# Kernel tuning notes

Hardware: AMD Instinct MI355X
Metric: run time of the kernel (lower is better)

Reference implementation:

```python
import jax, jax.numpy as jnp
import numpy as np

N_NODES = 50000
N_EDGES = 800000
N_GRAPHS = 128
HIDDEN = 64
HEADS = 2
OUT = 4
NEG_SLOPE = 0.2
ALPHA_FLAG = 0.05


def _gat_conv(x, src, dst, W, a_src, a_dst, b):
    # PyG GATConv, concat=False (mean over heads), self-loops already appended.
    N = x.shape[0]
    H, C = a_src.shape
    xh = (x @ W).reshape(N, H, C)                       # [N,H,C]
    s_src = (xh * a_src).sum(-1)                        # [N,H]
    s_dst = (xh * a_dst).sum(-1)                        # [N,H]
    e = s_src[src] + s_dst[dst]                         # [E,H]
    e = jnp.where(e > 0, e, NEG_SLOPE * e)              # LeakyReLU(0.2)
    emax = jax.ops.segment_max(e, dst, num_segments=N)  # per-dst softmax max
    emax = jnp.where(jnp.isfinite(emax), emax, 0.0)
    p = jnp.exp(e - emax[dst])
    denom = jax.ops.segment_sum(p, dst, num_segments=N)
    alpha = p / (denom[dst] + 1e-16)                    # [E,H]
    out = jax.ops.segment_sum(alpha[:, :, None] * xh[src], dst, num_segments=N)
    return out.mean(axis=1) + b                         # [N,HIDDEN]


def setup_inputs() -> dict:
    key = jax.random.key(0)
    ks = jax.random.split(key, 32)
    f = lambda k, shape, s=0.1: (jax.random.normal(k, shape) * s).astype(jnp.float32)
    inp = {}
    inp['x_all'] = jax.random.normal(ks[0], (N_NODES, 8), dtype=jnp.float32)
    inp['climber'] = jax.random.normal(ks[1], (N_GRAPHS, 4), dtype=jnp.float32)
    inp['edge_index'] = jax.random.randint(ks[2], (2, N_EDGES), 0, N_NODES)
    inp['batch'] = jnp.sort(jax.random.randint(ks[3], (N_NODES,), 0, N_GRAPHS))
    H = HIDDEN
    inp['W_in'] = f(ks[4], (6, H)); inp['b_in'] = jnp.zeros((H,), jnp.float32)
    inp['W_c'] = f(ks[5], (4, H)); inp['b_c'] = jnp.zeros((H,), jnp.float32)
    inp['W_f1'] = f(ks[6], (H, 2 * H)); inp['b_f1'] = jnp.zeros((2 * H,), jnp.float32)
    inp['W_f2'] = f(ks[7], (H, 2 * H)); inp['b_f2'] = jnp.zeros((2 * H,), jnp.float32)
    inp['W_g1'] = f(ks[8], (H, HEADS * H)); inp['a_src1'] = f(ks[9], (HEADS, H)); inp['a_dst1'] = f(ks[10], (HEADS, H)); inp['b_g1'] = jnp.zeros((H,), jnp.float32)
    inp['W_g2'] = f(ks[11], (H, HEADS * H)); inp['a_src2'] = f(ks[12], (HEADS, H)); inp['a_dst2'] = f(ks[13], (HEADS, H)); inp['b_g2'] = jnp.zeros((H,), jnp.float32)
    inp['W_cl1'] = f(ks[14], (H, H)); inp['b_cl1'] = jnp.zeros((H,), jnp.float32)
    inp['W_cl2'] = f(ks[15], (H, OUT)); inp['b_cl2'] = jnp.zeros((OUT,), jnp.float32)
    inp['W_fh1'] = f(ks[16], (2, 8), 0.001); inp['b_fh1'] = jnp.zeros((8,), jnp.float32)
    inp['W_fh2'] = f(ks[17], (8, OUT), 0.001); inp['b_fh2'] = jnp.zeros((OUT,), jnp.float32)
    return inp


def reference(x_all, climber, edge_index, batch, W_in, b_in, W_c, b_c,
              W_f1, b_f1, W_f2, b_f2,
              W_g1, a_src1, a_dst1, b_g1,
              W_g2, a_src2, a_dst2, b_g2,
              W_cl1, b_cl1, W_cl2, b_cl2,
              W_fh1, b_fh1, W_fh2, b_fh2):
    N = x_all.shape[0]
    flags = x_all[:, -2:]
    x = x_all[:, :-2]
    # climber embedding (eval mode -> dropout is identity)
    c = jax.nn.relu(climber @ W_c + b_c)                 # [G,H]
    x = x @ W_in + b_in                                  # [N,H]
    # FiLM 1
    gb = c @ W_f1 + b_f1
    gamma, beta = jnp.split(gb, 2, axis=-1)
    x = x * (1.0 + gamma[batch]) + beta[batch]
    # add self-loops (PyG GATConv default)
    loop = jnp.arange(N, dtype=edge_index.dtype)
    src = jnp.concatenate([edge_index[0], loop])
    dst = jnp.concatenate([edge_index[1], loop])
    x = jax.nn.relu(_gat_conv(x, src, dst, W_g1, a_src1, a_dst1, b_g1))
    # FiLM 2
    gb = c @ W_f2 + b_f2
    gamma, beta = jnp.split(gb, 2, axis=-1)
    x = x * (1.0 + gamma[batch]) + beta[batch]
    x = jax.nn.relu(_gat_conv(x, src, dst, W_g2, a_src2, a_dst2, b_g2))
    logits_main = jax.nn.relu(x @ W_cl1 + b_cl1) @ W_cl2 + b_cl2
    logits_flag = jax.nn.relu(flags @ W_fh1 + b_fh1) @ W_fh2 + b_fh2
    return logits_main + ALPHA_FLAG * logits_flag
```

## Files before the change

kernel.cpp:

```cpp
#include <hip/hip_runtime.h>
#include <hip/hip_fp16.h>

#define NEG_SLOPE 0.2f
#define ALPHA_FLAG 0.05f

typedef _Float16 h2t __attribute__((ext_vector_type(2)));
union h2u { unsigned u; h2t h; __half2 hh; float f; };
static __device__ __forceinline__ h2t u_as_h2(unsigned u) { h2u c; c.u = u; return c.h; }
static __device__ __forceinline__ float h2_as_f(__half2 h) { h2u c; c.hh = h; return c.f; }
static __device__ __forceinline__ h2t f_as_h2(float f) { h2u c; c.f = f; return c.h; }

static inline size_t align256(size_t x) { return (x + 255) & ~(size_t)255; }

__global__ void prep_kernel(const float* __restrict__ climber,
                            const float* __restrict__ W_c, const float* __restrict__ b_c,
                            const float* __restrict__ W_f1, const float* __restrict__ b_f1,
                            const float* __restrict__ W_f2, const float* __restrict__ b_f2,
                            float* __restrict__ gb1, float* __restrict__ gb2) {
    __shared__ float c_sh[64];
    int g = blockIdx.x, t = threadIdx.x;
    if (t < 64) {
        float acc = b_c[t];
#pragma unroll
        for (int k = 0; k < 4; ++k) acc = fmaf(climber[g * 4 + k], W_c[k * 64 + t], acc);
        c_sh[t] = fmaxf(acc, 0.f);
    }
    __syncthreads();
    float a1 = b_f1[t], a2 = b_f2[t];
#pragma unroll 8
    for (int h = 0; h < 64; ++h) {
        float cv = c_sh[h];
        a1 = fmaf(cv, W_f1[h * 128 + t], a1);
        a2 = fmaf(cv, W_f2[h * 128 + t], a2);
    }
    gb1[g * 128 + t] = a1;
    gb2[g * 128 + t] = a2;
}

__global__ void hist_kernel(const int* __restrict__ dst, int E,
                            int* __restrict__ counts, int* __restrict__ ranks) {
    int i4 = (blockIdx.x * blockDim.x + threadIdx.x) * 4;
    if (i4 + 3 < E) {
        int4 d = *(const int4*)&dst[i4];
        int4 r;
        r.x = atomicAdd(&counts[d.x], 1);
        r.y = atomicAdd(&counts[d.y], 1);
        r.z = atomicAdd(&counts[d.z], 1);
        r.w = atomicAdd(&counts[d.w], 1);
        *(int4*)&ranks[i4] = r;
    } else {
        for (int u = 0; u < 4; ++u)
            if (i4 + u < E) ranks[i4 + u] = atomicAdd(&counts[dst[i4 + u]], 1);
    }
}

#define SCAN_CHUNK 1024
__global__ void scan_kernel(const int* __restrict__ counts, int* __restrict__ row_ptr, int N) {
    __shared__ int sh[256];
    int b = blockIdx.x, t = threadIdx.x;
    int pre = 0;
    for (int i0 = t * 4; i0 < b * SCAN_CHUNK; i0 += 1024) {
        int4 v = *(const int4*)&counts[i0];
        pre += v.x + v.y + v.z + v.w + 4;
    }
    sh[t] = pre;
    __syncthreads();
#pragma unroll
    for (int off = 128; off; off >>= 1) {
        if (t < off) sh[t] += sh[t + off];
        __syncthreads();
    }
    int base = sh[0];
    __syncthreads();
    int idx0 = b * SCAN_CHUNK + t * 4;
    int c[4];
    if (idx0 + 3 < N) {
        int4 v = *(const int4*)&counts[idx0];
        c[0] = v.x + 1; c[1] = v.y + 1; c[2] = v.z + 1; c[3] = v.w + 1;
    } else {
#pragma unroll
        for (int u = 0; u < 4; ++u) c[u] = (idx0 + u < N) ? counts[idx0 + u] + 1 : 0;
    }
    int s = c[0] + c[1] + c[2] + c[3];
    sh[t] = s;
    __syncthreads();
#pragma unroll
    for (int off = 1; off < 256; off <<= 1) {
        int add = (t >= off) ? sh[t - off] : 0;
        __syncthreads();
        sh[t] += add;
        __syncthreads();
    }
    int run = base + sh[t] - s;
#pragma unroll
    for (int u = 0; u < 4; ++u) {
        if (idx0 + u < N) {
            row_ptr[idx0 + u] = run;
            run += c[u];
            if (idx0 + u == N - 1) row_ptr[N] = run;
        }
    }
}

__global__ void scatter_kernel(const int* __restrict__ src, const int* __restrict__ dst,
                               const int* __restrict__ ranks, const int* __restrict__ counts,
                               const int* __restrict__ row_ptr,
                               int Eh, int N, int* __restrict__ csr_src) {
    int t = blockIdx.x * blockDim.x + threadIdx.x;
    if (t < Eh) {
        int2 s2 = *(const int2*)&src[t * 2];
        int2 d2 = *(const int2*)&dst[t * 2];
        int2 r2 = *(const int2*)&ranks[t * 2];
        csr_src[row_ptr[d2.x] + r2.x] = s2.x;
        csr_src[row_ptr[d2.y] + r2.y] = s2.y;
    } else {
        int i = t - Eh;
        if (i < N) csr_src[row_ptr[i] + counts[i]] = i;
    }
}

#define XH_NB 32
__global__ __launch_bounds__(256, 4) void xh_kernel(
    const __half* __restrict__ xhalf, const float* __restrict__ W_g,
    const float* __restrict__ a_src, const float* __restrict__ a_dst,
    __half* __restrict__ xh, float* __restrict__ s_src, float* __restrict__ s_dst,
    int N, int in_mode,
    const float* __restrict__ x_all, const int* __restrict__ batch,
    const float* __restrict__ W_in, const float* __restrict__ b_in,
    const float* __restrict__ gb1) {
    __shared__ float x_sh[XH_NB * 64];
    __shared__ float win_sh[6 * 64 + 64];
    int t = threadIdx.x;
    int base = blockIdx.x * XH_NB;
    if (in_mode) {
        for (int i = t; i < 448; i += 256)
            win_sh[i] = (i < 384) ? W_in[i] : b_in[i - 384];
        __syncthreads();
        int nd = t >> 3;
        int jb = (t & 7) * 8;
        int n = base + nd;
        if (n < N) {
            float4 a = *(const float4*)&x_all[(size_t)n * 8];
            float2 b = *(const float2*)&x_all[(size_t)n * 8 + 4];
            float xa[6] = {a.x, a.y, a.z, a.w, b.x, b.y};
            int g = batch[n];
            const float* gbrow = &gb1[g * 128];
#pragma unroll
            for (int jj = 0; jj < 8; ++jj) {
                int j = jb + jj;
                float acc = win_sh[384 + j];
#pragma unroll
                for (int k = 0; k < 6; ++k) acc = fmaf(xa[k], win_sh[k * 64 + j], acc);
                x_sh[nd * 64 + j] = acc * (1.f + gbrow[j]) + gbrow[64 + j];
            }
        } else {
#pragma unroll
            for (int jj = 0; jj < 8; ++jj) x_sh[nd * 64 + jb + jj] = 0.f;
        }
    } else {
        int nvalid = N - base; if (nvalid > XH_NB) nvalid = XH_NB;
        int nhalves = nvalid * 64;
        int idx = t * 8;
        uint4 raw = make_uint4(0, 0, 0, 0);
        if (idx < nhalves) raw = *(const uint4*)&xhalf[(size_t)base * 64 + idx];
        float2 f0 = __half22float2(*(__half2*)&raw.x);
        float2 f1 = __half22float2(*(__half2*)&raw.y);
        float2 f2 = __half22float2(*(__half2*)&raw.z);
        float2 f3 = __half22float2(*(__half2*)&raw.w);
        x_sh[idx + 0] = f0.x; x_sh[idx + 1] = f0.y;
        x_sh[idx + 2] = f1.x; x_sh[idx + 3] = f1.y;
        x_sh[idx + 4] = f2.x; x_sh[idx + 5] = f2.y;
        x_sh[idx + 6] = f3.x; x_sh[idx + 7] = f3.y;
    }
    __syncthreads();
    int c = t & 63;
    int g = t >> 6;
    float acc0[8], acc1[8];
#pragma unroll
    for (int i = 0; i < 8; ++i) { acc0[i] = 0.f; acc1[i] = 0.f; }
    const float* W0 = W_g + c;
    const float* W1 = W_g + 64 + c;
#pragma unroll 2
    for (int k = 0; k < 64; k += 4) {
        float w0[4], w1[4];
#pragma unroll
        for (int u = 0; u < 4; ++u) { w0[u] = W0[(k + u) * 128]; w1[u] = W1[(k + u) * 128]; }
#pragma unroll
        for (int i = 0; i < 8; ++i) {
            float4 xv = *(const float4*)&x_sh[(g * 8 + i) * 64 + k];
            acc0[i] = fmaf(xv.x, w0[0], acc0[i]);
            acc0[i] = fmaf(xv.y, w0[1], acc0[i]);
            acc0[i] = fmaf(xv.z, w0[2], acc0[i]);
            acc0[i] = fmaf(xv.w, w0[3], acc0[i]);
            acc1[i] = fmaf(xv.x, w1[0], acc1[i]);
            acc1[i] = fmaf(xv.y, w1[1], acc1[i]);
            acc1[i] = fmaf(xv.z, w1[2], acc1[i]);
            acc1[i] = fmaf(xv.w, w1[3], acc1[i]);
        }
    }
    float as0 = a_src[c], ad0 = a_dst[c];
    float as1 = a_src[64 + c], ad1 = a_dst[64 + c];
#pragma unroll
    for (int i = 0; i < 8; ++i) {
        int n = base + g * 8 + i;
        float ps0 = acc0[i] * as0, pd0 = acc0[i] * ad0;
        float ps1 = acc1[i] * as1, pd1 = acc1[i] * ad1;
#pragma unroll
        for (int off = 32; off; off >>= 1) {
            ps0 += __shfl_xor(ps0, off); pd0 += __shfl_xor(pd0, off);
            ps1 += __shfl_xor(ps1, off); pd1 += __shfl_xor(pd1, off);
        }
        if (n < N) {
            if (c == 0) {
                s_src[n * 2 + 0] = ps0; s_src[n * 2 + 1] = ps1;
                s_dst[n * 2 + 0] = pd0; s_dst[n * 2 + 1] = pd1;
            }
            __half2 hv = __floats2half2_rn(acc0[i], acc1[i]);
            *(__half2*)&xh[(size_t)n * 128 + c * 2] = hv;
        }
    }
}

static __device__ __forceinline__ float dot2acc(unsigned xbits, h2t w, float acc) {
#if __has_builtin(__builtin_amdgcn_fdot2)
    return __builtin_amdgcn_fdot2(u_as_h2(xbits), w, acc, false);
#else
    h2u cx; cx.u = xbits;
    float2 xf = __half22float2(cx.hh);
    h2u cw; cw.h = w;
    float2 wf = __half22float2(cw.hh);
    return fmaf(xf.x, wf.x, fmaf(xf.y, wf.y, acc));
#endif
}

template <int MODE>
static __device__ __forceinline__ void agg_impl(
    const __half* __restrict__ xh, const float* __restrict__ s_src,
    const float* __restrict__ s_dst, const int* __restrict__ row_ptr,
    const int* __restrict__ csr_src, const float* __restrict__ b_g,
    const int* __restrict__ batch, const float* __restrict__ gb_film,
    __half* __restrict__ xout_h, int N,
    const float* __restrict__ x_all,
    const float* __restrict__ W_cl1, const float* __restrict__ b_cl1,
    const float* __restrict__ W_cl2, const float* __restrict__ b_cl2,
    const float* __restrict__ W_fh1, const float* __restrict__ b_fh1,
    const float* __restrict__ W_fh2, const float* __restrict__ b_fh2,
    float* __restrict__ out) {
    __shared__ float2 ps_sh[4][64];
    __shared__ float vh_sh[4][64];
    int lane = threadIdx.x & 63;
    int w = threadIdx.x >> 6;
    int n = (blockIdx.x * blockDim.x + threadIdx.x) >> 6;
    if (n >= N) return;
    int beg = row_ptr[n], end = row_ptr[n + 1];
    int deg = end - beg;
    float2 sd = *(const float2*)&s_dst[n * 2];
    const char* xhb = (const char*)xh;
    int sub = lane >> 4;
    unsigned q16 = (unsigned)(lane & 15) * 16u;
    float acc[4] = {0.f, 0.f, 0.f, 0.f};

    if (deg <= 64) {
        float p0 = 0.f, p1 = 0.f; unsigned sb = 0;
        if (lane < deg) {
            int s = csr_src[beg + lane];
            sb = (unsigned)s << 8;
            float2 ss = *(const float2*)&s_src[s * 2];
            float e0 = ss.x + sd.x, e1 = ss.y + sd.y;
            e0 = (e0 > 0.f) ? e0 : NEG_SLOPE * e0;
            e1 = (e1 > 0.f) ? e1 : NEG_SLOPE * e1;
            p0 = __expf(e0); p1 = __expf(e1);
        }
        float dp0 = p0, dp1 = p1;
#pragma unroll
        for (int off = 32; off; off >>= 1) {
            dp0 += __shfl_xor(dp0, off);
            dp1 += __shfl_xor(dp1, off);
        }
        float i0 = 0.5f / (dp0 + 1e-16f), i1 = 0.5f / (dp1 + 1e-16f);
        ps_sh[w][lane] = make_float2(h2_as_f(__floats2half2_rn(p0 * i0, p1 * i1)),
                                     __uint_as_float(sb));
        int mr = (deg + 3) & ~3;
#pragma unroll 4
        for (int j = 0; j < mr; j += 4) {
            float2 ps = ps_sh[w][j + sub];
            h2t wpk = f_as_h2(ps.x);
            unsigned voff = __float_as_uint(ps.y) + q16;
            uint4 hv = *(const uint4*)(xhb + voff);
            acc[0] = dot2acc(hv.x, wpk, acc[0]);
            acc[1] = dot2acc(hv.y, wpk, acc[1]);
            acc[2] = dot2acc(hv.z, wpk, acc[2]);
            acc[3] = dot2acc(hv.w, wpk, acc[3]);
        }
    } else {
        float dp0 = 0.f, dp1 = 0.f;
        for (int chunk = beg; chunk < end; chunk += 64) {
            int m = end - chunk; if (m > 64) m = 64;
            if (lane < m) {
                int s = csr_src[chunk + lane];
                float2 ss = *(const float2*)&s_src[s * 2];
                float e0 = ss.x + sd.x, e1 = ss.y + sd.y;
                e0 = (e0 > 0.f) ? e0 : NEG_SLOPE * e0;
                e1 = (e1 > 0.f) ? e1 : NEG_SLOPE * e1;
                dp0 += __expf(e0); dp1 += __expf(e1);
            }
        }
#pragma unroll
        for (int off = 32; off; off >>= 1) {
            dp0 += __shfl_xor(dp0, off);
            dp1 += __shfl_xor(dp1, off);
        }
        float i0 = 0.5f / (dp0 + 1e-16f), i1 = 0.5f / (dp1 + 1e-16f);
        for (int chunk = beg; chunk < end; chunk += 64) {
            int m = end - chunk; if (m > 64) m = 64;
            float p0 = 0.f, p1 = 0.f; unsigned sb = 0;
            if (lane < m) {
                int s = csr_src[chunk + lane];
                sb = (unsigned)s << 8;
                float2 ss = *(const float2*)&s_src[s * 2];
                float e0 = ss.x + sd.x, e1 = ss.y + sd.y;
                e0 = (e0 > 0.f) ? e0 : NEG_SLOPE * e0;
                e1 = (e1 > 0.f) ? e1 : NEG_SLOPE * e1;
                p0 = __expf(e0); p1 = __expf(e1);
            }
            ps_sh[w][lane] = make_float2(h2_as_f(__floats2half2_rn(p0 * i0, p1 * i1)),
                                         __uint_as_float(sb));
            int mr = (m + 3) & ~3;
#pragma unroll 4
            for (int j = 0; j < mr; j += 4) {
                float2 ps = ps_sh[w][j + sub];
                h2t wpk = f_as_h2(ps.x);
                unsigned voff = __float_as_uint(ps.y) + q16;
                uint4 hv = *(const uint4*)(xhb + voff);
                acc[0] = dot2acc(hv.x, wpk, acc[0]);
                acc[1] = dot2acc(hv.y, wpk, acc[1]);
                acc[2] = dot2acc(hv.z, wpk, acc[2]);
                acc[3] = dot2acc(hv.w, wpk, acc[3]);
            }
        }
    }
#pragma unroll
    for (int u = 0; u < 4; ++u) {
        acc[u] += __shfl_xor(acc[u], 16);
        acc[u] += __shfl_xor(acc[u], 32);
    }
    if (lane < 16) *(float4*)&vh_sh[w][lane * 4] = make_float4(acc[0], acc[1], acc[2], acc[3]);
    float v = vh_sh[w][lane] + b_g[lane];
    v = fmaxf(v, 0.f);
    if (MODE == 0) {
        int g = batch[n];
        v = v * (1.f + gb_film[g * 128 + lane]) + gb_film[g * 128 + 64 + lane];
        xout_h[(size_t)n * 64 + lane] = __float2half(v);
        return;
    }
    vh_sh[w][lane] = v;
    float h = b_cl1[lane];
#pragma unroll 4
    for (int k = 0; k < 64; k += 4) {
        float4 vq = *(const float4*)&vh_sh[w][k];
        h = fmaf(vq.x, W_cl1[(k + 0) * 64 + lane], h);
        h = fmaf(vq.y, W_cl1[(k + 1) * 64 + lane], h);
        h = fmaf(vq.z, W_cl1[(k + 2) * 64 + lane], h);
        h = fmaf(vq.w, W_cl1[(k + 3) * 64 + lane], h);
    }
    h = fmaxf(h, 0.f);
    float4 w2 = *(const float4*)&W_cl2[lane * 4];
    float o0 = h * w2.x, o1 = h * w2.y, o2 = h * w2.z, o3 = h * w2.w;
#pragma unroll
    for (int off = 32; off; off >>= 1) {
        o0 += __shfl_xor(o0, off); o1 += __shfl_xor(o1, off);
        o2 += __shfl_xor(o2, off); o3 += __shfl_xor(o3, off);
    }
    if (lane < 4) {
        float f0 = x_all[(size_t)n * 8 + 6], f1 = x_all[(size_t)n * 8 + 7];
        float lf = b_fh2[lane];
#pragma unroll
        for (int m = 0; m < 8; ++m) {
            float fm = fmaxf(fmaf(f0, W_fh1[m], fmaf(f1, W_fh1[8 + m], b_fh1[m])), 0.f);
            lf = fmaf(fm, W_fh2[m * 4 + lane], lf);
        }
        float om = (lane == 0) ? o0 : (lane == 1) ? o1 : (lane == 2) ? o2 : o3;
        out[(size_t)n * 4 + lane] = om + b_cl2[lane] + ALPHA_FLAG * lf;
    }
}

__global__ __launch_bounds__(256) void agg_film_kernel(
    const __half* xh, const float* s_src, const float* s_dst, const int* row_ptr,
    const int* csr_src, const float* b_g, const int* batch, const float* gb_film,
    __half* xout_h, int N) {
    agg_impl<0>(xh, s_src, s_dst, row_ptr, csr_src, b_g, batch, gb_film, xout_h, N,
                nullptr, nullptr, nullptr, nullptr, nullptr, nullptr, nullptr,
                nullptr, nullptr, nullptr);
}

__global__ __launch_bounds__(256) void agg_cls_kernel(
    const __half* xh, const float* s_src, const float* s_dst, const int* row_ptr,
    const int* csr_src, const float* b_g, int N, const float* x_all,
    const float* W_cl1, const float* b_cl1, const float* W_cl2, const float* b_cl2,
    const float* W_fh1, const float* b_fh1, const float* W_fh2, const float* b_fh2,
    float* out) {
    agg_impl<1>(xh, s_src, s_dst, row_ptr, csr_src, b_g, nullptr, nullptr, nullptr, N,
                x_all, W_cl1, b_cl1, W_cl2, b_cl2, W_fh1, b_fh1, W_fh2, b_fh2, out);
}

extern "C" void kernel_launch(void* const* d_in, const int* in_sizes, int n_in,
                              void* d_out, int out_size, void* d_ws, size_t ws_size,
                              hipStream_t stream) {
    const float* x_all   = (const float*)d_in[0];
    const float* climber = (const float*)d_in[1];
    const int*   eidx    = (const int*)d_in[2];
    const int*   batch   = (const int*)d_in[3];
    const float* W_in  = (const float*)d_in[4];
    const float* b_in  = (const float*)d_in[5];
    const float* W_c   = (const float*)d_in[6];
    const float* b_c   = (const float*)d_in[7];
    const float* W_f1  = (const float*)d_in[8];
    const float* b_f1  = (const float*)d_in[9];
    const float* W_f2  = (const float*)d_in[10];
    const float* b_f2  = (const float*)d_in[11];
    const float* W_g1  = (const float*)d_in[12];
    const float* a_s1  = (const float*)d_in[13];
    const float* a_d1  = (const float*)d_in[14];
    const float* b_g1  = (const float*)d_in[15];
    const float* W_g2  = (const float*)d_in[16];
    const float* a_s2  = (const float*)d_in[17];
    const float* a_d2  = (const float*)d_in[18];
    const float* b_g2  = (const float*)d_in[19];
    const float* W_cl1 = (const float*)d_in[20];
    const float* b_cl1 = (const float*)d_in[21];
    const float* W_cl2 = (const float*)d_in[22];
    const float* b_cl2 = (const float*)d_in[23];
    const float* W_fh1 = (const float*)d_in[24];
    const float* b_fh1 = (const float*)d_in[25];
    const float* W_fh2 = (const float*)d_in[26];
    const float* b_fh2 = (const float*)d_in[27];
    float* out = (float*)d_out;

    const int N = in_sizes[0] / 8;
    const int E = in_sizes[2] / 2;
    const int G = in_sizes[1] / 4;
    const int* src = eidx;
    const int* dst = eidx + E;
    const int NB_SCAN = (N + SCAN_CHUNK - 1) / SCAN_CHUNK;

    char* ws = (char*)d_ws;
    size_t off = 0;
    auto alloc = [&](size_t bytes) { char* p = ws + off; off += align256(bytes); return p; };
    float*  gb1     = (float*)alloc((size_t)G * 128 * 4);
    float*  gb2     = (float*)alloc((size_t)G * 128 * 4);
    __half* xbuf    = (__half*)alloc((size_t)N * 64 * 2);
    __half* xh      = (__half*)alloc((size_t)N * 128 * 2);
    float*  s_src   = (float*)alloc((size_t)N * 2 * 4);
    float*  s_dst   = (float*)alloc((size_t)N * 2 * 4);
    int*    counts  = (int*)alloc((size_t)N * 4);
    int*    ranks   = (int*)alloc((size_t)E * 4);
    int*    row_ptr = (int*)alloc((size_t)(N + 1) * 4);
    int*    csr_src = (int*)alloc((size_t)(E + N) * 4);
    (void)ws_size;

    prep_kernel<<<G, 128, 0, stream>>>(climber, W_c, b_c, W_f1, b_f1, W_f2, b_f2, gb1, gb2);
    hipMemsetAsync(counts, 0, (size_t)N * 4, stream);
    hist_kernel<<<(E / 4 + 255) / 256, 256, 0, stream>>>(dst, E, counts, ranks);
    scan_kernel<<<NB_SCAN, 256, 0, stream>>>(counts, row_ptr, N);
    scatter_kernel<<<(E / 2 + N + 255) / 256, 256, 0, stream>>>(src, dst, ranks, counts,
                                                                row_ptr, E / 2, N, csr_src);
    xh_kernel<<<(N + XH_NB - 1) / XH_NB, 256, 0, stream>>>(nullptr, W_g1, a_s1, a_d1, xh,
                                                           s_src, s_dst, N, 1,
                                                           x_all, batch, W_in, b_in, gb1);
    agg_film_kernel<<<(N * 64 + 255) / 256, 256, 0, stream>>>(xh, s_src, s_dst, row_ptr, csr_src,
                                                              b_g1, batch, gb2, xbuf, N);
    xh_kernel<<<(N + XH_NB - 1) / XH_NB, 256, 0, stream>>>(xbuf, W_g2, a_s2, a_d2, xh,
                                                           s_src, s_dst, N, 0,
                                                           nullptr, nullptr, nullptr, nullptr, nullptr);
    agg_cls_kernel<<<(N * 64 + 255) / 256, 256, 0, stream>>>(xh, s_src, s_dst, row_ptr, csr_src,
                                                             b_g2, N, x_all, W_cl1, b_cl1,
                                                             W_cl2, b_cl2, W_fh1, b_fh1,
                                                             W_fh2, b_fh2, out);
}
```

Measured before the change: 223.7 us.

## Process two destination nodes per wavefront in GAT aggregation kernels

Each 64-lane wavefront now aggregates two destination nodes (n and n+N/2) at once, interleaving their gathers and dot2 accumulations so more independent memory loads are in flight per wave. The grid is halved, which amortises per-wave setup such as the row_ptr reads and the classifier weight loads. In exchange the inner loop runs to the larger of the two degrees, so lanes idle when the degrees differ. Register and LDS use per wave also grow, which may lower occupancy.

Result: no change. 220.7 us (-1.3%).

```diff
diff --git a/kernel.cpp b/kernel.cpp
--- a/kernel.cpp
+++ b/kernel.cpp
@@ -233,37 +233,34 @@
 #endif
 }
 
-template <int MODE>
-static __device__ __forceinline__ void agg_impl(
-    const __half* __restrict__ xh, const float* __restrict__ s_src,
-    const float* __restrict__ s_dst, const int* __restrict__ row_ptr,
-    const int* __restrict__ csr_src, const float* __restrict__ b_g,
-    const int* __restrict__ batch, const float* __restrict__ gb_film,
-    __half* __restrict__ xout_h, int N,
-    const float* __restrict__ x_all,
-    const float* __restrict__ W_cl1, const float* __restrict__ b_cl1,
-    const float* __restrict__ W_cl2, const float* __restrict__ b_cl2,
-    const float* __restrict__ W_fh1, const float* __restrict__ b_fh1,
-    const float* __restrict__ W_fh2, const float* __restrict__ b_fh2,
-    float* __restrict__ out) {
-    __shared__ float2 ps_sh[4][64];
-    __shared__ float vh_sh[4][64];
-    int lane = threadIdx.x & 63;
-    int w = threadIdx.x >> 6;
-    int n = (blockIdx.x * blockDim.x + threadIdx.x) >> 6;
-    if (n >= N) return;
-    int beg = row_ptr[n], end = row_ptr[n + 1];
-    int deg = end - beg;
-    float2 sd = *(const float2*)&s_dst[n * 2];
-    const char* xhb = (const char*)xh;
-    int sub = lane >> 4;
-    unsigned q16 = (unsigned)(lane & 15) * 16u;
-    float acc[4] = {0.f, 0.f, 0.f, 0.f};
-
-    if (deg <= 64) {
+static __device__ __forceinline__ void agg_one_slow(
+    const char* __restrict__ xhb, const float* __restrict__ s_src,
+    float2 sd, const int* __restrict__ csr_src, int beg, int end,
+    int lane, int sub, unsigned q16, float2* __restrict__ ps_slot,
+    float acc[4]) {
+    float dp0 = 0.f, dp1 = 0.f;
+    for (int chunk = beg; chunk < end; chunk += 64) {
+        int m = end - chunk; if (m > 64) m = 64;
+        if (lane < m) {
+            int s = csr_src[chunk + lane];
+            float2 ss = *(const float2*)&s_src[s * 2];
+            float e0 = ss.x + sd.x, e1 = ss.y + sd.y;
+            e0 = (e0 > 0.f) ? e0 : NEG_SLOPE * e0;
+            e1 = (e1 > 0.f) ? e1 : NEG_SLOPE * e1;
+            dp0 += __expf(e0); dp1 += __expf(e1);
+        }
+    }
+#pragma unroll
+    for (int off = 32; off; off >>= 1) {
+        dp0 += __shfl_xor(dp0, off);
+        dp1 += __shfl_xor(dp1, off);
+    }
+    float i0 = 0.5f / (dp0 + 1e-16f), i1 = 0.5f / (dp1 + 1e-16f);
+    for (int chunk = beg; chunk < end; chunk += 64) {
+        int m = end - chunk; if (m > 64) m = 64;
         float p0 = 0.f, p1 = 0.f; unsigned sb = 0;
-        if (lane < deg) {
-            int s = csr_src[beg + lane];
+        if (lane < m) {
+            int s = csr_src[chunk + lane];
             sb = (unsigned)s << 8;
             float2 ss = *(const float2*)&s_src[s * 2];
             float e0 = ss.x + sd.x, e1 = ss.y + sd.y;
@@ -271,19 +268,12 @@
             e1 = (e1 > 0.f) ? e1 : NEG_SLOPE * e1;
             p0 = __expf(e0); p1 = __expf(e1);
         }
-        float dp0 = p0, dp1 = p1;
-#pragma unroll
-        for (int off = 32; off; off >>= 1) {
-            dp0 += __shfl_xor(dp0, off);
-            dp1 += __shfl_xor(dp1, off);
-        }
-        float i0 = 0.5f / (dp0 + 1e-16f), i1 = 0.5f / (dp1 + 1e-16f);
-        ps_sh[w][lane] = make_float2(h2_as_f(__floats2half2_rn(p0 * i0, p1 * i1)),
-                                     __uint_as_float(sb));
-        int mr = (deg + 3) & ~3;
+        ps_slot[lane] = make_float2(h2_as_f(__floats2half2_rn(p0 * i0, p1 * i1)),
+                                    __uint_as_float(sb));
+        int mr = (m + 3) & ~3;
 #pragma unroll 4
         for (int j = 0; j < mr; j += 4) {
-            float2 ps = ps_sh[w][j + sub];
+            float2 ps = ps_slot[j + sub];
             h2t wpk = f_as_h2(ps.x);
             unsigned voff = __float_as_uint(ps.y) + q16;
             uint4 hv = *(const uint4*)(xhb + voff);
@@ -292,114 +282,180 @@
             acc[2] = dot2acc(hv.z, wpk, acc[2]);
             acc[3] = dot2acc(hv.w, wpk, acc[3]);
         }
+    }
+}
+
+template <int MODE>
+static __device__ __forceinline__ void agg_impl(
+    const __half* __restrict__ xh, const float* __restrict__ s_src,
+    const float* __restrict__ s_dst, const int* __restrict__ row_ptr,
+    const int* __restrict__ csr_src, const float* __restrict__ b_g,
+    const int* __restrict__ batch, const float* __restrict__ gb_film,
+    __half* __restrict__ xout_h, int N, int half,
+    const float* __restrict__ x_all,
+    const float* __restrict__ W_cl1, const float* __restrict__ b_cl1,
+    const float* __restrict__ W_cl2, const float* __restrict__ b_cl2,
+    const float* __restrict__ W_fh1, const float* __restrict__ b_fh1,
+    const float* __restrict__ W_fh2, const float* __restrict__ b_fh2,
+    float* __restrict__ out) {
+    __shared__ float2 ps_sh[4][2][64];
+    __shared__ float vh_sh[4][2][64];
+    int lane = threadIdx.x & 63;
+    int w = threadIdx.x >> 6;
+    int n0 = (blockIdx.x * blockDim.x + threadIdx.x) >> 6;
+    if (n0 >= half) return;
+    int n1 = n0 + half;
+    bool valid1 = n1 < N;
+    const char* xhb = (const char*)xh;
+    int sub = lane >> 4;
+    unsigned q16 = (unsigned)(lane & 15) * 16u;
+    float accA[4] = {0.f, 0.f, 0.f, 0.f};
+    float accB[4] = {0.f, 0.f, 0.f, 0.f};
+
+    int begA = row_ptr[n0], endA = row_ptr[n0 + 1];
+    int begB = valid1 ? row_ptr[n1] : 0, endB = valid1 ? row_ptr[n1 + 1] : 0;
+    int degA = endA - begA, degB = endB - begB;
+    float2 sdA = *(const float2*)&s_dst[n0 * 2];
+    float2 sdB = valid1 ? *(const float2*)&s_dst[n1 * 2] : make_float2(0.f, 0.f);
+
+    if (degA <= 64 && degB <= 64) {
+        int sA = (lane < degA) ? csr_src[begA + lane] : -1;
+        int sB = (lane < degB) ? csr_src[begB + lane] : -1;
+        float2 ssA = (sA >= 0) ? *(const float2*)&s_src[sA * 2] : make_float2(0.f, 0.f);
+        float2 ssB = (sB >= 0) ? *(const float2*)&s_src[sB * 2] : make_float2(0.f, 0.f);
+        float pA0 = 0.f, pA1 = 0.f, pB0 = 0.f, pB1 = 0.f;
+        unsigned sbA = 0, sbB = 0;
+        if (sA >= 0) {
+            sbA = (unsigned)sA << 8;
+            float e0 = ssA.x + sdA.x, e1 = ssA.y + sdA.y;
+            e0 = (e0 > 0.f) ? e0 : NEG_SLOPE * e0;
+            e1 = (e1 > 0.f) ? e1 : NEG_SLOPE * e1;
+            pA0 = __expf(e0); pA1 = __expf(e1);
+        }
+        if (sB >= 0) {
+            sbB = (unsigned)sB << 8;
+            float e0 = ssB.x + sdB.x, e1 = ssB.y + sdB.y;
+            e0 = (e0 > 0.f) ? e0 : NEG_SLOPE * e0;
+            e1 = (e1 > 0.f) ? e1 : NEG_SLOPE * e1;
+            pB0 = __expf(e0); pB1 = __expf(e1);
+        }
+        float dA0 = pA0, dA1 = pA1, dB0 = pB0, dB1 = pB1;
+#pragma unroll
+        for (int off = 32; off; off >>= 1) {
+            dA0 += __shfl_xor(dA0, off); dA1 += __shfl_xor(dA1, off);
+            dB0 += __shfl_xor(dB0, off); dB1 += __shfl_xor(dB1, off);
+        }
+        float iA0 = 0.5f / (dA0 + 1e-16f), iA1 = 0.5f / (dA1 + 1e-16f);
+        float iB0 = 0.5f / (dB0 + 1e-16f), iB1 = 0.5f / (dB1 + 1e-16f);
+        ps_sh[w][0][lane] = make_float2(h2_as_f(__floats2half2_rn(pA0 * iA0, pA1 * iA1)),
+                                        __uint_as_float(sbA));
+        ps_sh[w][1][lane] = make_float2(h2_as_f(__floats2half2_rn(pB0 * iB0, pB1 * iB1)),
+                                        __uint_as_float(sbB));
+        int mrA = (degA + 3) & ~3, mrB = (degB + 3) & ~3;
+        int mr = mrA > mrB ? mrA : mrB;
+#pragma unroll 2
+        for (int j = 0; j < mr; j += 4) {
+            float2 psA = ps_sh[w][0][j + sub];
+            float2 psB = ps_sh[w][1][j + sub];
+            unsigned voA = __float_as_uint(psA.y) + q16;
+            unsigned voB = __float_as_uint(psB.y) + q16;
+            uint4 hvA = *(const uint4*)(xhb + voA);
+            uint4 hvB = *(const uint4*)(xhb + voB);
+            h2t wA = f_as_h2(psA.x), wB = f_as_h2(psB.x);
+            accA[0] = dot2acc(hvA.x, wA, accA[0]);
+            accA[1] = dot2acc(hvA.y, wA, accA[1]);
+            accA[2] = dot2acc(hvA.z, wA, accA[2]);
+            accA[3] = dot2acc(hvA.w, wA, accA[3]);
+            accB[0] = dot2acc(hvB.x, wB, accB[0]);
+            accB[1] = dot2acc(hvB.y, wB, accB[1]);
+            accB[2] = dot2acc(hvB.z, wB, accB[2]);
+            accB[3] = dot2acc(hvB.w, wB, accB[3]);
+        }
     } else {
-        float dp0 = 0.f, dp1 = 0.f;
-        for (int chunk = beg; chunk < end; chunk += 64) {
-            int m = end - chunk; if (m > 64) m = 64;
-            if (lane < m) {
-                int s = csr_src[chunk + lane];
-                float2 ss = *(const float2*)&s_src[s * 2];
-                float e0 = ss.x + sd.x, e1 = ss.y + sd.y;
-                e0 = (e0 > 0.f) ? e0 : NEG_SLOPE * e0;
-                e1 = (e1 > 0.f) ? e1 : NEG_SLOPE * e1;
-                dp0 += __expf(e0); dp1 += __expf(e1);
+        agg_one_slow(xhb, s_src, sdA, csr_src, begA, endA, lane, sub, q16,
+                     &ps_sh[w][0][0], accA);
+        if (valid1)
+            agg_one_slow(xhb, s_src, sdB, csr_src, begB, endB, lane, sub, q16,
+                         &ps_sh[w][1][0], accB);
+    }
+#pragma unroll
+    for (int u = 0; u < 4; ++u) {
+        accA[u] += __shfl_xor(accA[u], 16);
+        accA[u] += __shfl_xor(accA[u], 32);
+        accB[u] += __shfl_xor(accB[u], 16);
+        accB[u] += __shfl_xor(accB[u], 32);
+    }
+    if (lane < 16) {
+        *(float4*)&vh_sh[w][0][lane * 4] = make_float4(accA[0], accA[1], accA[2], accA[3]);
+        *(float4*)&vh_sh[w][1][lane * 4] = make_float4(accB[0], accB[1], accB[2], accB[3]);
+    }
+    float bg = b_g[lane];
+    float vA = fmaxf(vh_sh[w][0][lane] + bg, 0.f);
+    float vB = fmaxf(vh_sh[w][1][lane] + bg, 0.f);
+    if (MODE == 0) {
+        int gA = batch[n0];
+        vA = vA * (1.f + gb_film[gA * 128 + lane]) + gb_film[gA * 128 + 64 + lane];
+        xout_h[(size_t)n0 * 64 + lane] = __float2half(vA);
+        if (valid1) {
+            int gB = batch[n1];
+            vB = vB * (1.f + gb_film[gB * 128 + lane]) + gb_film[gB * 128 + 64 + lane];
+            xout_h[(size_t)n1 * 64 + lane] = __float2half(vB);
+        }
+        return;
+    }
+    vh_sh[w][0][lane] = vA;
+    vh_sh[w][1][lane] = vB;
+    float4 w2 = *(const float4*)&W_cl2[lane * 4];
+    float b1v = b_cl1[lane];
+    for (int q = 0; q < 2; ++q) {
+        int n = q ? n1 : n0;
+        if (q && !valid1) break;
+        float h = b1v;
+#pragma unroll 4
+        for (int k = 0; k < 64; k += 4) {
+            float4 vq = *(const float4*)&vh_sh[w][q][k];
+            h = fmaf(vq.x, W_cl1[(k + 0) * 64 + lane], h);
+            h = fmaf(vq.y, W_cl1[(k + 1) * 64 + lane], h);
+            h = fmaf(vq.z, W_cl1[(k + 2) * 64 + lane], h);
+            h = fmaf(vq.w, W_cl1[(k + 3) * 64 + lane], h);
+        }
+        h = fmaxf(h, 0.f);
+        float o0 = h * w2.x, o1 = h * w2.y, o2 = h * w2.z, o3 = h * w2.w;
+#pragma unroll
+        for (int off = 32; off; off >>= 1) {
+            o0 += __shfl_xor(o0, off); o1 += __shfl_xor(o1, off);
+            o2 += __shfl_xor(o2, off); o3 += __shfl_xor(o3, off);
+        }
+        if (lane < 4) {
+            float f0 = x_all[(size_t)n * 8 + 6], f1 = x_all[(size_t)n * 8 + 7];
+            float lf = b_fh2[lane];
+#pragma unroll
+            for (int m = 0; m < 8; ++m) {
+                float fm = fmaxf(fmaf(f0, W_fh1[m], fmaf(f1, W_fh1[8 + m], b_fh1[m])), 0.f);
+                lf = fmaf(fm, W_fh2[m * 4 + lane], lf);
             }
-        }
-#pragma unroll
-        for (int off = 32; off; off >>= 1) {
-            dp0 += __shfl_xor(dp0, off);
-            dp1 += __shfl_xor(dp1, off);
-        }
-        float i0 = 0.5f / (dp0 + 1e-16f), i1 = 0.5f / (dp1 + 1e-16f);
-        for (int chunk = beg; chunk < end; chunk += 64) {
-            int m = end - chunk; if (m > 64) m = 64;
-            float p0 = 0.f, p1 = 0.f; unsigned sb = 0;
-            if (lane < m) {
-                int s = csr_src[chunk + lane];
-                sb = (unsigned)s << 8;
-                float2 ss = *(const float2*)&s_src[s * 2];
-                float e0 = ss.x + sd.x, e1 = ss.y + sd.y;
-                e0 = (e0 > 0.f) ? e0 : NEG_SLOPE * e0;
-                e1 = (e1 > 0.f) ? e1 : NEG_SLOPE * e1;
-                p0 = __expf(e0); p1 = __expf(e1);
-            }
-            ps_sh[w][lane] = make_float2(h2_as_f(__floats2half2_rn(p0 * i0, p1 * i1)),
-                                         __uint_as_float(sb));
-            int mr = (m + 3) & ~3;
-#pragma unroll 4
-            for (int j = 0; j < mr; j += 4) {
-                float2 ps = ps_sh[w][j + sub];
-                h2t wpk = f_as_h2(ps.x);
-                unsigned voff = __float_as_uint(ps.y) + q16;
-                uint4 hv = *(const uint4*)(xhb + voff);
-                acc[0] = dot2acc(hv.x, wpk, acc[0]);
-                acc[1] = dot2acc(hv.y, wpk, acc[1]);
-                acc[2] = dot2acc(hv.z, wpk, acc[2]);
-                acc[3] = dot2acc(hv.w, wpk, acc[3]);
-            }
-        }
-    }
-#pragma unroll
-    for (int u = 0; u < 4; ++u) {
-        acc[u] += __shfl_xor(acc[u], 16);
-        acc[u] += __shfl_xor(acc[u], 32);
-    }
-    if (lane < 16) *(float4*)&vh_sh[w][lane * 4] = make_float4(acc[0], acc[1], acc[2], acc[3]);
-    float v = vh_sh[w][lane] + b_g[lane];
-    v = fmaxf(v, 0.f);
-    if (MODE == 0) {
-        int g = batch[n];
-        v = v * (1.f + gb_film[g * 128 + lane]) + gb_film[g * 128 + 64 + lane];
-        xout_h[(size_t)n * 64 + lane] = __float2half(v);
-        return;
-    }
-    vh_sh[w][lane] = v;
-    float h = b_cl1[lane];
-#pragma unroll 4
-    for (int k = 0; k < 64; k += 4) {
-        float4 vq = *(const float4*)&vh_sh[w][k];
-        h = fmaf(vq.x, W_cl1[(k + 0) * 64 + lane], h);
-        h = fmaf(vq.y, W_cl1[(k + 1) * 64 + lane], h);
-        h = fmaf(vq.z, W_cl1[(k + 2) * 64 + lane], h);
-        h = fmaf(vq.w, W_cl1[(k + 3) * 64 + lane], h);
-    }
-    h = fmaxf(h, 0.f);
-    float4 w2 = *(const float4*)&W_cl2[lane * 4];
-    float o0 = h * w2.x, o1 = h * w2.y, o2 = h * w2.z, o3 = h * w2.w;
-#pragma unroll
-    for (int off = 32; off; off >>= 1) {
-        o0 += __shfl_xor(o0, off); o1 += __shfl_xor(o1, off);
-        o2 += __shfl_xor(o2, off); o3 += __shfl_xor(o3, off);
-    }
-    if (lane < 4) {
-        float f0 = x_all[(size_t)n * 8 + 6], f1 = x_all[(size_t)n * 8 + 7];
-        float lf = b_fh2[lane];
-#pragma unroll
-        for (int m = 0; m < 8; ++m) {
-            float fm = fmaxf(fmaf(f0, W_fh1[m], fmaf(f1, W_fh1[8 + m], b_fh1[m])), 0.f);
-            lf = fmaf(fm, W_fh2[m * 4 + lane], lf);
-        }
-        float om = (lane == 0) ? o0 : (lane == 1) ? o1 : (lane == 2) ? o2 : o3;
-        out[(size_t)n * 4 + lane] = om + b_cl2[lane] + ALPHA_FLAG * lf;
+            float om = (lane == 0) ? o0 : (lane == 1) ? o1 : (lane == 2) ? o2 : o3;
+            out[(size_t)n * 4 + lane] = om + b_cl2[lane] + ALPHA_FLAG * lf;
+        }
     }
 }
 
 __global__ __launch_bounds__(256) void agg_film_kernel(
     const __half* xh, const float* s_src, const float* s_dst, const int* row_ptr,
     const int* csr_src, const float* b_g, const int* batch, const float* gb_film,
-    __half* xout_h, int N) {
-    agg_impl<0>(xh, s_src, s_dst, row_ptr, csr_src, b_g, batch, gb_film, xout_h, N,
+    __half* xout_h, int N, int half) {
+    agg_impl<0>(xh, s_src, s_dst, row_ptr, csr_src, b_g, batch, gb_film, xout_h, N, half,
                 nullptr, nullptr, nullptr, nullptr, nullptr, nullptr, nullptr,
                 nullptr, nullptr, nullptr);
 }
 
 __global__ __launch_bounds__(256) void agg_cls_kernel(
     const __half* xh, const float* s_src, const float* s_dst, const int* row_ptr,
-    const int* csr_src, const float* b_g, int N, const float* x_all,
+    const int* csr_src, const float* b_g, int N, int half, const float* x_all,
     const float* W_cl1, const float* b_cl1, const float* W_cl2, const float* b_cl2,
     const float* W_fh1, const float* b_fh1, const float* W_fh2, const float* b_fh2,
     float* out) {
-    agg_impl<1>(xh, s_src, s_dst, row_ptr, csr_src, b_g, nullptr, nullptr, nullptr, N,
+    agg_impl<1>(xh, s_src, s_dst, row_ptr, csr_src, b_g, nullptr, nullptr, nullptr, N, half,
                 x_all, W_cl1, b_cl1, W_cl2, b_cl2, W_fh1, b_fh1, W_fh2, b_fh2, out);
 }
 
@@ -442,6 +498,7 @@
     const int* src = eidx;
     const int* dst = eidx + E;
     const int NB_SCAN = (N + SCAN_CHUNK - 1) / SCAN_CHUNK;
+    const int half = (N + 1) / 2;
 
     char* ws = (char*)d_ws;
     size_t off = 0;
@@ -467,13 +524,14 @@
     xh_kernel<<<(N + XH_NB - 1) / XH_NB, 256, 0, stream>>>(nullptr, W_g1, a_s1, a_d1, xh,
                                                            s_src, s_dst, N, 1,
                                                            x_all, batch, W_in, b_in, gb1);
-    agg_film_kernel<<<(N * 64 + 255) / 256, 256, 0, stream>>>(xh, s_src, s_dst, row_ptr, csr_src,
-                                                              b_g1, batch, gb2, xbuf, N);
+    agg_film_kernel<<<(half * 64 + 255) / 256, 256, 0, stream>>>(xh, s_src, s_dst, row_ptr,
+                                                                 csr_src, b_g1, batch, gb2,
+                                                                 xbuf, N, half);
     xh_kernel<<<(N + XH_NB - 1) / XH_NB, 256, 0, stream>>>(xbuf, W_g2, a_s2, a_d2, xh,
                                                            s_src, s_dst, N, 0,
                                                            nullptr, nullptr, nullptr, nullptr, nullptr);
-    agg_cls_kernel<<<(N * 64 + 255) / 256, 256, 0, stream>>>(xh, s_src, s_dst, row_ptr, csr_src,
-                                                             b_g2, N, x_all, W_cl1, b_cl1,
-                                                             W_cl2, b_cl2, W_fh1, b_fh1,
-                                                             W_fh2, b_fh2, out);
-}
+    agg_cls_kernel<<<(half * 64 + 255) / 256, 256, 0, stream>>>(xh, s_src, s_dst, row_ptr,
+                                                                csr_src, b_g2, N, half, x_all,
+                                                                W_cl1, b_cl1, W_cl2, b_cl2,
+                                                                W_fh1, b_fh1, W_fh2, b_fh2, out);
+}
```
